# Optimization experiments

Measured on AMD Instinct MI355X. Metric: run time of the kernel, lower is better.

Reference implementation:

```python
import jax, jax.numpy as jnp
import numpy as np

EMBED = 1024
HEADS = 16
HEAD_DIM = EMBED // HEADS


def setup_inputs() -> dict:
    key = jax.random.key(0)
    ks = jax.random.split(key, 7)
    N, S = 2, 2048
    k = jax.random.normal(ks[0], (N, S, EMBED), dtype=jnp.float32)
    q = jax.random.normal(ks[1], (N, S, EMBED), dtype=jnp.float32)
    v = jax.random.normal(ks[2], (N, S, EMBED), dtype=jnp.float32)
    sc = 1.0 / np.sqrt(HEAD_DIM)
    # nn.Linear weights, applied as x @ W.T
    Wk = jax.random.normal(ks[3], (HEAD_DIM, HEAD_DIM), dtype=jnp.float32) * sc
    Wq = jax.random.normal(ks[4], (HEAD_DIM, HEAD_DIM), dtype=jnp.float32) * sc
    Wv = jax.random.normal(ks[5], (HEAD_DIM, HEAD_DIM), dtype=jnp.float32) * sc
    Wo = jax.random.normal(ks[6], (EMBED, EMBED), dtype=jnp.float32) / np.sqrt(EMBED)
    return {"k": k, "q": q, "v": v, "Wk": Wk, "Wq": Wq, "Wv": Wv, "Wo": Wo}


def reference(k, q, v, Wk, Wq, Wv, Wo):
    N, S, _ = q.shape
    # reshape to [N, S, H, D]; per-head projection weights shared across heads
    kh = jnp.einsum('nshd,ed->nshe', k.reshape(N, S, HEADS, HEAD_DIM), Wk)
    qh = jnp.einsum('nshd,ed->nshe', q.reshape(N, S, HEADS, HEAD_DIM), Wq)
    vh = jnp.einsum('nshd,ed->nshe', v.reshape(N, S, HEADS, HEAD_DIM), Wv)
    # energy: [N, H, q_len, k_len]
    energy = jnp.einsum('nqhd,nkhd->nhqk', qh, kh)
    attn = jax.nn.softmax(energy / jnp.sqrt(jnp.float32(HEAD_DIM)), axis=-1)
    out = jnp.einsum('nhqk,nkhd->nqhd', attn, vh).reshape(N, S, EMBED)
    return out @ Wo.T
```

## Files before the change

kernel.cpp:

```cpp
#include <hip/hip_runtime.h>

#define SQ   2048
#define HEADS 16
#define HD   64
#define EMB  1024

typedef __attribute__((ext_vector_type(2))) __fp16 h2;
typedef __attribute__((ext_vector_type(4))) __fp16 h4;
typedef __attribute__((ext_vector_type(8))) __fp16 h8;
typedef __attribute__((ext_vector_type(4))) float f4;
typedef unsigned short USH;
typedef unsigned int   UI;

__device__ __forceinline__ UI pkh(float a, float b) {
    h2 v = __builtin_amdgcn_cvt_pkrtz(a, b);
    return __builtin_bit_cast(UI, v);
}

__device__ __forceinline__ void glds16(const void* g, void* l) {
    __builtin_amdgcn_global_load_lds(
        (const __attribute__((address_space(1))) unsigned int*)g,
        (__attribute__((address_space(3))) unsigned int*)l, 16, 0, 0);
}

__global__ __launch_bounds__(256) void proj_fused(
    const float* __restrict__ q_in, const float* __restrict__ k_in,
    const float* __restrict__ v_in, const float* __restrict__ Wq,
    const float* __restrict__ Wk,   const float* __restrict__ Wv,
    const float* __restrict__ Wo,
    USH* __restrict__ Qh, USH* __restrict__ Kh, USH* __restrict__ Vh,
    USH* __restrict__ Wob)
{
    int t = threadIdx.x;
    if (blockIdx.y == 3) {
        int i = blockIdx.x * 256 + t;
        for (int j = 0; j < 4; ++j) {
            float4 v = ((const float4*)Wo)[i + j * 65536];
            uint2 pk; pk.x = pkh(v.x, v.y); pk.y = pkh(v.z, v.w);
            *(uint2*)(Wob + ((size_t)i + (size_t)j * 65536) * 4) = pk;
        }
        return;
    }
    const float* X = (blockIdx.y == 0) ? q_in : (blockIdx.y == 1) ? k_in : v_in;
    const float* W = (blockIdx.y == 0) ? Wq   : (blockIdx.y == 1) ? Wk   : Wv;
    USH* Out       = (blockIdx.y == 0) ? Qh   : (blockIdx.y == 1) ? Kh   : Vh;
    float scale    = (blockIdx.y == 0) ? 0.18033688011112043f : 1.0f;

    __shared__ __align__(16) USH Xl[256][72];
    __shared__ __align__(16) USH Wl[64][72];

    const float4* Xg = (const float4*)(X + (size_t)blockIdx.x * 16384);
    for (int j = 0; j < 16; ++j) {
        int f = t + j * 256;
        float4 v = Xg[f];
        int row = f >> 4; int col = (f & 15) << 2;
        uint2 pk; pk.x = pkh(v.x, v.y); pk.y = pkh(v.z, v.w);
        *(uint2*)&Xl[row][col] = pk;
    }
    const float4* Wg = (const float4*)W;
    for (int j = 0; j < 4; ++j) {
        int f = t + j * 256;
        float4 v = Wg[f];
        int row = f >> 4; int col = (f & 15) << 2;
        uint2 pk; pk.x = pkh(v.x, v.y); pk.y = pkh(v.z, v.w);
        *(uint2*)&Wl[row][col] = pk;
    }
    __syncthreads();

    int wv = t >> 6, lane = t & 63, l4 = lane & 15, quad = lane >> 4;

    h8 wf[4][2], xf[4][2];
    for (int et = 0; et < 4; ++et)
        for (int ks = 0; ks < 2; ++ks)
            wf[et][ks] = *(const h8*)&Wl[et * 16 + l4][ks * 32 + quad * 8];
    for (int rt = 0; rt < 4; ++rt)
        for (int ks = 0; ks < 2; ++ks)
            xf[rt][ks] = *(const h8*)&Xl[wv * 64 + rt * 16 + l4][ks * 32 + quad * 8];

    f4 acc[4][4];
    for (int et = 0; et < 4; ++et)
        for (int rt = 0; rt < 4; ++rt) acc[et][rt] = (f4)(0.0f);
    for (int et = 0; et < 4; ++et)
        for (int rt = 0; rt < 4; ++rt)
            for (int ks = 0; ks < 2; ++ks)
                acc[et][rt] = __builtin_amdgcn_mfma_f32_16x16x32_f16(
                    wf[et][ks], xf[rt][ks], acc[et][rt], 0, 0, 0);

    for (int rt = 0; rt < 4; ++rt) {
        int ns = blockIdx.x * 16 + wv * 4 + rt;
        int n = ns >> 11, s = ns & 2047;
        USH* ob = Out + (((size_t)(n * HEADS) + l4) * SQ + s) * HD;
        for (int et = 0; et < 4; ++et) {
            uint2 pk;
            pk.x = pkh(acc[et][rt][0] * scale, acc[et][rt][1] * scale);
            pk.y = pkh(acc[et][rt][2] * scale, acc[et][rt][3] * scale);
            *(uint2*)(ob + et * 16 + quad * 4) = pk;
        }
    }
}

__global__ __launch_bounds__(256) void vtrans(const USH* __restrict__ Vh,
                                              USH* __restrict__ Vt)
{
    __shared__ __align__(16) USH L[64][72];
    int t = threadIdx.x;
    int nh = blockIdx.y, s0 = blockIdx.x * 64;
    int row = t >> 2, c = (t & 3) * 16;
    const USH* src = Vh + ((size_t)nh * SQ + s0) * HD;
    *(uint4*)&L[row][c]     = *(const uint4*)(src + (size_t)row * HD + c);
    *(uint4*)&L[row][c + 8] = *(const uint4*)(src + (size_t)row * HD + c + 8);
    __syncthreads();
    UI wbuf[8];
#pragma unroll
    for (int j = 0; j < 8; ++j)
        wbuf[j] = (UI)L[c + 2 * j][row] | ((UI)L[c + 2 * j + 1][row] << 16);
    uint4 o0, o1;
    o0.x = wbuf[0]; o0.y = wbuf[1]; o0.z = wbuf[2]; o0.w = wbuf[3];
    o1.x = wbuf[4]; o1.y = wbuf[5]; o1.z = wbuf[6]; o1.w = wbuf[7];
    USH* dst = Vt + ((size_t)nh * HD + row) * SQ + s0 + c;
    *(uint4*)dst = o0;
    *(uint4*)(dst + 8) = o1;
}

__global__ __launch_bounds__(256, 3) void attn_kernel(
    const USH* __restrict__ Qh, const USH* __restrict__ Kh,
    const USH* __restrict__ Vt, USH* __restrict__ Oh)
{
    __shared__ union {
        struct { USH K[512 * 8]; USH V[512 * 8]; USH Q[64][72]; } s;
        struct { float Osum[64][68]; float Lsum[64]; } r;
    } lds;

    int t = threadIdx.x, w = t >> 6, lane = t & 63;
    int l4 = lane & 15, quad = lane >> 4;
    int b = blockIdx.x;
    int nh = b & 31;
    int q0 = (b >> 5) * 64;
    const USH* Qg = Qh + ((size_t)nh * SQ + q0) * HD;
    const USH* Kg = Kh + (size_t)nh * SQ * HD;
    const USH* Vg = Vt + (size_t)nh * HD * SQ;

    {
        int srow = t >> 2, scol = (t & 3) * 16;
        *(uint4*)&lds.s.Q[srow][scol]     = *(const uint4*)(Qg + (size_t)srow * HD + scol);
        *(uint4*)&lds.s.Q[srow][scol + 8] = *(const uint4*)(Qg + (size_t)srow * HD + scol + 8);
    }
    __syncthreads();
    h8 bq[4][2];
    for (int qt = 0; qt < 4; ++qt)
        for (int ks = 0; ks < 2; ++ks)
            bq[qt][ks] = *(const h8*)&lds.s.Q[qt * 16 + l4][ks * 32 + quad * 8];

    f4 o[4][4];
    for (int dt = 0; dt < 4; ++dt)
        for (int qt = 0; qt < 4; ++qt) o[dt][qt] = (f4)(0.0f);
    float lsum[4] = {0.f, 0.f, 0.f, 0.f};

    int key = w * 16 + l4;
    int kslot0 = key * 8 + (quad ^ (key & 7));
    int kslot1 = key * 8 + ((4 + quad) ^ (key & 7));
    int dchunk = w * 2 + (quad >> 1);
    int vhalf = (quad & 1) * 4;

    for (int kt = 0; kt < SQ / 64; ++kt) {
        __syncthreads();
#pragma unroll
        for (int j = 0; j < 2; ++j) {
            int s = j * 256 + t, r = s >> 3, c = (s & 7) ^ (r & 7);
            glds16(Kg + (size_t)kt * 4096 + r * 64 + c * 8, lds.s.K + s * 8);
        }
#pragma unroll
        for (int j = 0; j < 2; ++j) {
            int s = j * 256 + t, r = s >> 3, c = (s & 7) ^ (r & 7);
            glds16(Vg + (size_t)r * SQ + kt * 64 + c * 8, lds.s.V + s * 8);
        }
        __syncthreads();

        h8 ak0 = *(const h8*)(lds.s.K + kslot0 * 8);
        h8 ak1 = *(const h8*)(lds.s.K + kslot1 * 8);
        f4 sc[4];
#pragma unroll
        for (int qt = 0; qt < 4; ++qt) sc[qt] = (f4)(0.0f);
#pragma unroll
        for (int qt = 0; qt < 4; ++qt)
            sc[qt] = __builtin_amdgcn_mfma_f32_16x16x32_f16(ak0, bq[qt][0], sc[qt], 0, 0, 0);
#pragma unroll
        for (int qt = 0; qt < 4; ++qt)
            sc[qt] = __builtin_amdgcn_mfma_f32_16x16x32_f16(ak1, bq[qt][1], sc[qt], 0, 0, 0);

        h4 av[4];
#pragma unroll
        for (int dt = 0; dt < 4; ++dt) {
            int d = dt * 16 + l4;
            int vs = d * 8 + (dchunk ^ (d & 7));
            av[dt] = *(const h4*)(lds.s.V + vs * 8 + vhalf);
        }

        h4 p[4];
#pragma unroll
        for (int qt = 0; qt < 4; ++qt) {
            float p0 = __builtin_amdgcn_exp2f(sc[qt][0]);
            float p1 = __builtin_amdgcn_exp2f(sc[qt][1]);
            float p2 = __builtin_amdgcn_exp2f(sc[qt][2]);
            float p3 = __builtin_amdgcn_exp2f(sc[qt][3]);
            lsum[qt] += (p0 + p1) + (p2 + p3);
            uint2 u; u.x = pkh(p0, p1); u.y = pkh(p2, p3);
            p[qt] = __builtin_bit_cast(h4, u);
        }
#pragma unroll
        for (int dt = 0; dt < 4; ++dt)
#pragma unroll
            for (int qt = 0; qt < 4; ++qt)
                o[dt][qt] = __builtin_amdgcn_mfma_f32_16x16x16f16(
                    av[dt], p[qt], o[dt][qt], 0, 0, 0);
    }

#pragma unroll
    for (int qt = 0; qt < 4; ++qt) {
        lsum[qt] += __shfl_xor(lsum[qt], 16, 64);
        lsum[qt] += __shfl_xor(lsum[qt], 32, 64);
    }

    __syncthreads();
    for (int ph = 0; ph < 4; ++ph) {
        if (w == ph) {
            for (int dt = 0; dt < 4; ++dt)
                for (int qt = 0; qt < 4; ++qt) {
                    float* dst = &lds.r.Osum[qt * 16 + l4][dt * 16 + quad * 4];
                    f4 val = o[dt][qt];
                    if (ph) val += *(const f4*)dst;
                    *(f4*)dst = val;
                }
            if (quad == 0)
                for (int qt = 0; qt < 4; ++qt) {
                    int qi = qt * 16 + l4;
                    lds.r.Lsum[qi] = ph ? (lds.r.Lsum[qi] + lsum[qt]) : lsum[qt];
                }
        }
        __syncthreads();
    }

    int n = nh >> 4, h = nh & 15;
    int q = t >> 2, d0 = (t & 3) * 16;
    float inv = 1.0f / lds.r.Lsum[q];
    float vv[16];
#pragma unroll
    for (int i = 0; i < 4; ++i) {
        f4 x = *(const f4*)&lds.r.Osum[q][d0 + i * 4];
        vv[i * 4 + 0] = x[0] * inv; vv[i * 4 + 1] = x[1] * inv;
        vv[i * 4 + 2] = x[2] * inv; vv[i * 4 + 3] = x[3] * inv;
    }
    uint4 ou0, ou1;
    ou0.x = pkh(vv[0], vv[1]);   ou0.y = pkh(vv[2], vv[3]);
    ou0.z = pkh(vv[4], vv[5]);   ou0.w = pkh(vv[6], vv[7]);
    ou1.x = pkh(vv[8], vv[9]);   ou1.y = pkh(vv[10], vv[11]);
    ou1.z = pkh(vv[12], vv[13]); ou1.w = pkh(vv[14], vv[15]);
    USH* ob = Oh + ((size_t)(n * SQ + q0 + q)) * EMB + h * HD + d0;
    *(uint4*)ob = ou0;
    *(uint4*)(ob + 8) = ou1;
}

__global__ __launch_bounds__(256, 4) void gemm_bt(const USH* __restrict__ A,
                                                  const USH* __restrict__ B,
                                                  float* __restrict__ C)
{
    __shared__ __align__(16) USH Al[1024 * 8];
    __shared__ __align__(16) USH Bl[512 * 8];
    int t = threadIdx.x, w = t >> 6, lane = t & 63;
    int l4 = lane & 15, quad = lane >> 4;
    int m0 = blockIdx.y * 128, n0 = blockIdx.x * 64;
    int wm = (w >> 1) * 64, wn = (w & 1) * 32;

    f4 acc[4][2];
    for (int mt = 0; mt < 4; ++mt)
        for (int nt = 0; nt < 2; ++nt) acc[mt][nt] = (f4)(0.0f);

    int aslot[4][2], bslot[2][2];
#pragma unroll
    for (int mt = 0; mt < 4; ++mt)
#pragma unroll
        for (int ks = 0; ks < 2; ++ks) {
            int m = wm + mt * 16 + l4;
            aslot[mt][ks] = m * 8 + ((ks * 4 + quad) ^ (m & 7));
        }
#pragma unroll
    for (int nt = 0; nt < 2; ++nt)
#pragma unroll
        for (int ks = 0; ks < 2; ++ks) {
            int nn = wn + nt * 16 + l4;
            bslot[nt][ks] = nn * 8 + ((ks * 4 + quad) ^ (nn & 7));
        }

    for (int k0 = 0; k0 < 1024; k0 += 64) {
        __syncthreads();
#pragma unroll
        for (int j = 0; j < 4; ++j) {
            int s = j * 256 + t, r = s >> 3, c = (s & 7) ^ (r & 7);
            glds16(A + (size_t)(m0 + r) * 1024 + k0 + c * 8, Al + s * 8);
        }
#pragma unroll
        for (int j = 0; j < 2; ++j) {
            int s = j * 256 + t, r = s >> 3, c = (s & 7) ^ (r & 7);
            glds16(B + (size_t)(n0 + r) * 1024 + k0 + c * 8, Bl + s * 8);
        }
        __syncthreads();

        h8 a[4][2], bf[2][2];
#pragma unroll
        for (int mt = 0; mt < 4; ++mt)
#pragma unroll
            for (int ks = 0; ks < 2; ++ks)
                a[mt][ks] = *(const h8*)(Al + aslot[mt][ks] * 8);
#pragma unroll
        for (int nt = 0; nt < 2; ++nt)
#pragma unroll
            for (int ks = 0; ks < 2; ++ks)
                bf[nt][ks] = *(const h8*)(Bl + bslot[nt][ks] * 8);
#pragma unroll
        for (int mt = 0; mt < 4; ++mt)
#pragma unroll
            for (int nt = 0; nt < 2; ++nt)
#pragma unroll
                for (int ks = 0; ks < 2; ++ks)
                    acc[mt][nt] = __builtin_amdgcn_mfma_f32_16x16x32_f16(
                        a[mt][ks], bf[nt][ks], acc[mt][nt], 0, 0, 0);
    }

    for (int mt = 0; mt < 4; ++mt)
        for (int nt = 0; nt < 2; ++nt)
            for (int r = 0; r < 4; ++r)
                C[(size_t)(m0 + wm + mt * 16 + quad * 4 + r) * 1024 +
                  (n0 + wn + nt * 16 + l4)] = acc[mt][nt][r];
}

extern "C" void kernel_launch(void* const* d_in, const int* in_sizes, int n_in,
                              void* d_out, int out_size, void* d_ws, size_t ws_size,
                              hipStream_t stream) {
    const float* k_in = (const float*)d_in[0];
    const float* q_in = (const float*)d_in[1];
    const float* v_in = (const float*)d_in[2];
    const float* Wk   = (const float*)d_in[3];
    const float* Wq   = (const float*)d_in[4];
    const float* Wv   = (const float*)d_in[5];
    const float* Wo   = (const float*)d_in[6];
    float* out = (float*)d_out;

    char* ws = (char*)d_ws;
    USH* Qh  = (USH*)(ws);
    USH* Kh  = (USH*)(ws + 8388608);
    USH* Vh  = (USH*)(ws + 16777216);
    USH* Vt  = (USH*)(ws + 25165824);
    USH* Oh  = (USH*)(ws + 33554432);
    USH* Wob = (USH*)(ws + 41943040);

    proj_fused<<<dim3(256, 4), dim3(256), 0, stream>>>(
        q_in, k_in, v_in, Wq, Wk, Wv, Wo, Qh, Kh, Vh, Wob);
    vtrans<<<dim3(32, 32), dim3(256), 0, stream>>>(Vh, Vt);
    attn_kernel<<<dim3(1024), dim3(256), 0, stream>>>(Qh, Kh, Vt, Oh);
    gemm_bt<<<dim3(16, 32), dim3(256), 0, stream>>>(Oh, Wob, out);
}
```

Baseline: 187.3 us.

## Fuse V transpose into projection and load K/V straight to registers in attention

The V projection now writes its output directly in transposed [nh][d][s] layout, which removes the separate vtrans kernel launch and its extra pass over V. The attention kernel drops LDS staging of Q, K and V and the two barriers per key tile. Each wave instead reads its own K fragment (prefetched one tile ahead) and its V fragments directly from global memory. This cuts synchronisation and LDS traffic but relies on L2 to serve the K/V reads, which may now be less coalesced and issued redundantly across blocks. Because four waves split the keys and each touches a distinct subset, the re-read count is unchanged.

```diff
diff --git a/kernel.cpp b/kernel.cpp
--- a/kernel.cpp
+++ b/kernel.cpp
@@ -28,7 +28,7 @@
     const float* __restrict__ v_in, const float* __restrict__ Wq,
     const float* __restrict__ Wk,   const float* __restrict__ Wv,
     const float* __restrict__ Wo,
-    USH* __restrict__ Qh, USH* __restrict__ Kh, USH* __restrict__ Vh,
+    USH* __restrict__ Qh, USH* __restrict__ Kh, USH* __restrict__ Vt,
     USH* __restrict__ Wob)
 {
     int t = threadIdx.x;
@@ -43,7 +43,6 @@
     }
     const float* X = (blockIdx.y == 0) ? q_in : (blockIdx.y == 1) ? k_in : v_in;
     const float* W = (blockIdx.y == 0) ? Wq   : (blockIdx.y == 1) ? Wk   : Wv;
-    USH* Out       = (blockIdx.y == 0) ? Qh   : (blockIdx.y == 1) ? Kh   : Vh;
     float scale    = (blockIdx.y == 0) ? 0.18033688011112043f : 1.0f;
 
     __shared__ __align__(16) USH Xl[256][72];
@@ -86,50 +85,38 @@
                 acc[et][rt] = __builtin_amdgcn_mfma_f32_16x16x32_f16(
                     wf[et][ks], xf[rt][ks], acc[et][rt], 0, 0, 0);
 
-    for (int rt = 0; rt < 4; ++rt) {
-        int ns = blockIdx.x * 16 + wv * 4 + rt;
-        int n = ns >> 11, s = ns & 2047;
-        USH* ob = Out + (((size_t)(n * HEADS) + l4) * SQ + s) * HD;
-        for (int et = 0; et < 4; ++et) {
-            uint2 pk;
-            pk.x = pkh(acc[et][rt][0] * scale, acc[et][rt][1] * scale);
-            pk.y = pkh(acc[et][rt][2] * scale, acc[et][rt][3] * scale);
-            *(uint2*)(ob + et * 16 + quad * 4) = pk;
-        }
-    }
-}
-
-__global__ __launch_bounds__(256) void vtrans(const USH* __restrict__ Vh,
-                                              USH* __restrict__ Vt)
-{
-    __shared__ __align__(16) USH L[64][72];
-    int t = threadIdx.x;
-    int nh = blockIdx.y, s0 = blockIdx.x * 64;
-    int row = t >> 2, c = (t & 3) * 16;
-    const USH* src = Vh + ((size_t)nh * SQ + s0) * HD;
-    *(uint4*)&L[row][c]     = *(const uint4*)(src + (size_t)row * HD + c);
-    *(uint4*)&L[row][c + 8] = *(const uint4*)(src + (size_t)row * HD + c + 8);
-    __syncthreads();
-    UI wbuf[8];
-#pragma unroll
-    for (int j = 0; j < 8; ++j)
-        wbuf[j] = (UI)L[c + 2 * j][row] | ((UI)L[c + 2 * j + 1][row] << 16);
-    uint4 o0, o1;
-    o0.x = wbuf[0]; o0.y = wbuf[1]; o0.z = wbuf[2]; o0.w = wbuf[3];
-    o1.x = wbuf[4]; o1.y = wbuf[5]; o1.z = wbuf[6]; o1.w = wbuf[7];
-    USH* dst = Vt + ((size_t)nh * HD + row) * SQ + s0 + c;
-    *(uint4*)dst = o0;
-    *(uint4*)(dst + 8) = o1;
+    if (blockIdx.y == 2) {
+        int ns0 = blockIdx.x * 16 + wv * 4;
+        int n = ns0 >> 11, s = ns0 & 2047;
+        for (int et = 0; et < 4; ++et)
+            for (int j = 0; j < 4; ++j) {
+                int e = et * 16 + quad * 4 + j;
+                uint2 pk;
+                pk.x = pkh(acc[et][0][j], acc[et][1][j]);
+                pk.y = pkh(acc[et][2][j], acc[et][3][j]);
+                *(uint2*)(Vt + (((size_t)(n * HEADS + l4) * HD + e) * SQ + s)) = pk;
+            }
+    } else {
+        USH* Out = (blockIdx.y == 0) ? Qh : Kh;
+        for (int rt = 0; rt < 4; ++rt) {
+            int ns = blockIdx.x * 16 + wv * 4 + rt;
+            int n = ns >> 11, s = ns & 2047;
+            USH* ob = Out + (((size_t)(n * HEADS) + l4) * SQ + s) * HD;
+            for (int et = 0; et < 4; ++et) {
+                uint2 pk;
+                pk.x = pkh(acc[et][rt][0] * scale, acc[et][rt][1] * scale);
+                pk.y = pkh(acc[et][rt][2] * scale, acc[et][rt][3] * scale);
+                *(uint2*)(ob + et * 16 + quad * 4) = pk;
+            }
+        }
+    }
 }
 
 __global__ __launch_bounds__(256, 3) void attn_kernel(
     const USH* __restrict__ Qh, const USH* __restrict__ Kh,
     const USH* __restrict__ Vt, USH* __restrict__ Oh)
 {
-    __shared__ union {
-        struct { USH K[512 * 8]; USH V[512 * 8]; USH Q[64][72]; } s;
-        struct { float Osum[64][68]; float Lsum[64]; } r;
-    } lds;
+    __shared__ struct { float Osum[64][68]; float Lsum[64]; } red;
 
     int t = threadIdx.x, w = t >> 6, lane = t & 63;
     int l4 = lane & 15, quad = lane >> 4;
@@ -140,61 +127,43 @@
     const USH* Kg = Kh + (size_t)nh * SQ * HD;
     const USH* Vg = Vt + (size_t)nh * HD * SQ;
 
-    {
-        int srow = t >> 2, scol = (t & 3) * 16;
-        *(uint4*)&lds.s.Q[srow][scol]     = *(const uint4*)(Qg + (size_t)srow * HD + scol);
-        *(uint4*)&lds.s.Q[srow][scol + 8] = *(const uint4*)(Qg + (size_t)srow * HD + scol + 8);
-    }
-    __syncthreads();
     h8 bq[4][2];
+#pragma unroll
     for (int qt = 0; qt < 4; ++qt)
+#pragma unroll
         for (int ks = 0; ks < 2; ++ks)
-            bq[qt][ks] = *(const h8*)&lds.s.Q[qt * 16 + l4][ks * 32 + quad * 8];
+            bq[qt][ks] = *(const h8*)(Qg + (size_t)(qt * 16 + l4) * HD + ks * 32 + quad * 8);
 
     f4 o[4][4];
+#pragma unroll
     for (int dt = 0; dt < 4; ++dt)
+#pragma unroll
         for (int qt = 0; qt < 4; ++qt) o[dt][qt] = (f4)(0.0f);
     float lsum[4] = {0.f, 0.f, 0.f, 0.f};
 
-    int key = w * 16 + l4;
-    int kslot0 = key * 8 + (quad ^ (key & 7));
-    int kslot1 = key * 8 + ((4 + quad) ^ (key & 7));
-    int dchunk = w * 2 + (quad >> 1);
-    int vhalf = (quad & 1) * 4;
-
+    const USH* kbase = Kg + (size_t)(w * 16 + l4) * HD;
+    const USH* vbase = Vg + (size_t)l4 * SQ + w * 16 + quad * 4;
+
+    h8 ak0 = *(const h8*)(kbase + quad * 8);
+    h8 ak1 = *(const h8*)(kbase + 32 + quad * 8);
+
+#pragma unroll 1
     for (int kt = 0; kt < SQ / 64; ++kt) {
-        __syncthreads();
-#pragma unroll
-        for (int j = 0; j < 2; ++j) {
-            int s = j * 256 + t, r = s >> 3, c = (s & 7) ^ (r & 7);
-            glds16(Kg + (size_t)kt * 4096 + r * 64 + c * 8, lds.s.K + s * 8);
-        }
-#pragma unroll
-        for (int j = 0; j < 2; ++j) {
-            int s = j * 256 + t, r = s >> 3, c = (s & 7) ^ (r & 7);
-            glds16(Vg + (size_t)r * SQ + kt * 64 + c * 8, lds.s.V + s * 8);
-        }
-        __syncthreads();
-
-        h8 ak0 = *(const h8*)(lds.s.K + kslot0 * 8);
-        h8 ak1 = *(const h8*)(lds.s.K + kslot1 * 8);
         f4 sc[4];
 #pragma unroll
-        for (int qt = 0; qt < 4; ++qt) sc[qt] = (f4)(0.0f);
-#pragma unroll
-        for (int qt = 0; qt < 4; ++qt)
-            sc[qt] = __builtin_amdgcn_mfma_f32_16x16x32_f16(ak0, bq[qt][0], sc[qt], 0, 0, 0);
-#pragma unroll
-        for (int qt = 0; qt < 4; ++qt)
-            sc[qt] = __builtin_amdgcn_mfma_f32_16x16x32_f16(ak1, bq[qt][1], sc[qt], 0, 0, 0);
+        for (int qt = 0; qt < 4; ++qt) {
+            f4 s = __builtin_amdgcn_mfma_f32_16x16x32_f16(ak0, bq[qt][0], (f4)(0.0f), 0, 0, 0);
+            sc[qt] = __builtin_amdgcn_mfma_f32_16x16x32_f16(ak1, bq[qt][1], s, 0, 0, 0);
+        }
+
+        int ktn = (kt + 1) & 31;
+        h8 nk0 = *(const h8*)(kbase + (size_t)ktn * 4096 + quad * 8);
+        h8 nk1 = *(const h8*)(kbase + (size_t)ktn * 4096 + 32 + quad * 8);
 
         h4 av[4];
 #pragma unroll
-        for (int dt = 0; dt < 4; ++dt) {
-            int d = dt * 16 + l4;
-            int vs = d * 8 + (dchunk ^ (d & 7));
-            av[dt] = *(const h4*)(lds.s.V + vs * 8 + vhalf);
-        }
+        for (int dt = 0; dt < 4; ++dt)
+            av[dt] = *(const h4*)(vbase + (size_t)dt * 16 * SQ + kt * 64);
 
         h4 p[4];
 #pragma unroll
@@ -207,12 +176,15 @@
             uint2 u; u.x = pkh(p0, p1); u.y = pkh(p2, p3);
             p[qt] = __builtin_bit_cast(h4, u);
         }
+
 #pragma unroll
         for (int dt = 0; dt < 4; ++dt)
 #pragma unroll
             for (int qt = 0; qt < 4; ++qt)
                 o[dt][qt] = __builtin_amdgcn_mfma_f32_16x16x16f16(
                     av[dt], p[qt], o[dt][qt], 0, 0, 0);
+
+        ak0 = nk0; ak1 = nk1;
     }
 
 #pragma unroll
@@ -226,7 +198,7 @@
         if (w == ph) {
             for (int dt = 0; dt < 4; ++dt)
                 for (int qt = 0; qt < 4; ++qt) {
-                    float* dst = &lds.r.Osum[qt * 16 + l4][dt * 16 + quad * 4];
+                    float* dst = &red.Osum[qt * 16 + l4][dt * 16 + quad * 4];
                     f4 val = o[dt][qt];
                     if (ph) val += *(const f4*)dst;
                     *(f4*)dst = val;
@@ -234,7 +206,7 @@
             if (quad == 0)
                 for (int qt = 0; qt < 4; ++qt) {
                     int qi = qt * 16 + l4;
-                    lds.r.Lsum[qi] = ph ? (lds.r.Lsum[qi] + lsum[qt]) : lsum[qt];
+                    red.Lsum[qi] = ph ? (red.Lsum[qi] + lsum[qt]) : lsum[qt];
                 }
         }
         __syncthreads();
@@ -242,11 +214,11 @@
 
     int n = nh >> 4, h = nh & 15;
     int q = t >> 2, d0 = (t & 3) * 16;
-    float inv = 1.0f / lds.r.Lsum[q];
+    float inv = 1.0f / red.Lsum[q];
     float vv[16];
 #pragma unroll
     for (int i = 0; i < 4; ++i) {
-        f4 x = *(const f4*)&lds.r.Osum[q][d0 + i * 4];
+        f4 x = *(const f4*)&red.Osum[q][d0 + i * 4];
         vv[i * 4 + 0] = x[0] * inv; vv[i * 4 + 1] = x[1] * inv;
         vv[i * 4 + 2] = x[2] * inv; vv[i * 4 + 3] = x[3] * inv;
     }
@@ -348,14 +320,12 @@
     char* ws = (char*)d_ws;
     USH* Qh  = (USH*)(ws);
     USH* Kh  = (USH*)(ws + 8388608);
-    USH* Vh  = (USH*)(ws + 16777216);
-    USH* Vt  = (USH*)(ws + 25165824);
-    USH* Oh  = (USH*)(ws + 33554432);
-    USH* Wob = (USH*)(ws + 41943040);
+    USH* Vt  = (USH*)(ws + 16777216);
+    USH* Oh  = (USH*)(ws + 25165824);
+    USH* Wob = (USH*)(ws + 33554432);
 
     proj_fused<<<dim3(256, 4), dim3(256), 0, stream>>>(
-        q_in, k_in, v_in, Wq, Wk, Wv, Wo, Qh, Kh, Vh, Wob);
-    vtrans<<<dim3(32, 32), dim3(256), 0, stream>>>(Vh, Vt);
+        q_in, k_in, v_in, Wq, Wk, Wv, Wo, Qh, Kh, Vt, Wob);
     attn_kernel<<<dim3(1024), dim3(256), 0, stream>>>(Qh, Kh, Vt, Oh);
     gemm_bt<<<dim3(16, 32), dim3(256), 0, stream>>>(Oh, Wob, out);
 }
```

Result: slower. 218.6 us (+16.7%).
